# Optimization experiments

Hardware: AMD Instinct MI355X
Metric: run time of the kernel (lower is better)

## Reference

```python
import jax, jax.numpy as jnp
import numpy as np

B, S, D, H = 2, 4096, 512, 8
DH = D // H  # head dim = 64

def setup_inputs() -> dict:
    key = jax.random.key(0)
    ks = jax.random.split(key, 9)
    s = 0.02
    return {
        "Q": jax.random.normal(ks[0], (B, S, D), jnp.float32),
        "Wq": jax.random.normal(ks[1], (D, D), jnp.float32) * s,
        "bq": jnp.zeros((D,), jnp.float32),
        "Wk": jax.random.normal(ks[2], (D, D), jnp.float32) * s,
        "bk": jnp.zeros((D,), jnp.float32),
        "Wv": jax.random.normal(ks[3], (D, D), jnp.float32) * s,
        "bv": jnp.zeros((D,), jnp.float32),
        "Wo": jax.random.normal(ks[4], (D, D), jnp.float32) * s,
        "bo": jnp.zeros((D,), jnp.float32),
    }

def reference(Q, Wq, bq, Wk, bk, Wv, bv, Wo, bo):
    bs, s, d = Q.shape
    scale = DH ** -0.5
    # torch Linear: x @ W.T + b, W is [out, in]
    q = (Q @ Wq.T + bq).reshape(bs, s, H, DH).transpose(0, 2, 1, 3)  # [b,h,s,dh]
    k = (Q @ Wk.T + bk).reshape(bs, s, H, DH).transpose(0, 2, 1, 3)
    v = (Q @ Wv.T + bv).reshape(bs, s, H, DH).transpose(0, 2, 1, 3)
    scores = jnp.einsum('bhqd,bhkd->bhqk', q, k) * scale  # [b,h,s,s]
    attn = jax.nn.softmax(scores, axis=-1)
    out = jnp.einsum('bhqk,bhkd->bhqd', attn, v)  # [b,h,s,dh]
    out = out.transpose(0, 2, 1, 3).reshape(bs, s, H * DH)
    out = out @ Wo.T + bo
    return (out, attn)
```

## Files before the change

kernel.cpp:

```cpp
#include <hip/hip_runtime.h>
#include <hip/hip_bf16.h>

#define B_  2
#define S_  4096
#define D_  512
#define H_  8
#define DH_ 64
#define BH_ 16
#define M_  (B_*S_)

typedef __attribute__((ext_vector_type(4))) float f32x4;
typedef __attribute__((ext_vector_type(8))) short s16x8;
typedef __attribute__((ext_vector_type(4))) short s16x4;

#define MFMA(A,Bv,C) __builtin_amdgcn_mfma_f32_16x16x32_bf16(A,Bv,C,0,0,0)

typedef const void __attribute__((address_space(1)))* gas_t;
typedef void __attribute__((address_space(3)))* las_t;
#define GLDS(gp, lp) __builtin_amdgcn_global_load_lds((gas_t)(gp), (las_t)(lp), 16, 0, 0)

#define EXP_C 0.18033688011112042f

static __device__ __forceinline__ unsigned short f2bf(float f){
    union { float f; unsigned int u; } v; v.f = f;
    unsigned int r = (v.u + 0x7FFFu + ((v.u >> 16) & 1u)) >> 16;
    return (unsigned short)r;
}
static __device__ __forceinline__ float bf2f(unsigned short b){
    union { unsigned int u; float f; } v; v.u = ((unsigned int)b) << 16;
    return v.f;
}

__global__ __launch_bounds__(256) void cvt_bf16(const float* __restrict__ src,
                                                unsigned short* __restrict__ dst, int n4){
    int i = blockIdx.x * 256 + threadIdx.x;
    if (i < n4){
        float4 v = reinterpret_cast<const float4*>(src)[i];
        ushort4 o;
        o.x = f2bf(v.x); o.y = f2bf(v.y); o.z = f2bf(v.z); o.w = f2bf(v.w);
        reinterpret_cast<ushort4*>(dst)[i] = o;
    }
}

__global__ __launch_bounds__(256) void cvt_w4(const float* __restrict__ s0, const float* __restrict__ s1,
                                              const float* __restrict__ s2, const float* __restrict__ s3,
                                              unsigned short* __restrict__ d0, unsigned short* __restrict__ d1,
                                              unsigned short* __restrict__ d2, unsigned short* __restrict__ d3){
    const float* s; unsigned short* d;
    switch (blockIdx.y){
        case 0: s = s0; d = d0; break;
        case 1: s = s1; d = d1; break;
        case 2: s = s2; d = d2; break;
        default: s = s3; d = d3; break;
    }
    int i = blockIdx.x * 256 + threadIdx.x;
    float4 v = reinterpret_cast<const float4*>(s)[i];
    ushort4 o;
    o.x = f2bf(v.x); o.y = f2bf(v.y); o.z = f2bf(v.z); o.w = f2bf(v.w);
    reinterpret_cast<ushort4*>(d)[i] = o;
}

__global__ __launch_bounds__(256) void gemm_bt(const unsigned short* __restrict__ A,
                                               const unsigned short* __restrict__ W,
                                               const float* __restrict__ bias,
                                               unsigned short* __restrict__ dst_bf,
                                               float* __restrict__ dst_f32){
    const int mt = blockIdx.x, nt0 = blockIdx.y;
    const int wave = threadIdx.x >> 6, lane = threadIdx.x & 63;
    const int g = lane >> 4, r16 = lane & 15;
    const unsigned short* Ap = A + (size_t)(mt*64 + wave*16 + r16) * 512;

    f32x4 acc[4];
    #pragma unroll
    for (int i = 0; i < 4; ++i) acc[i] = (f32x4){0.f,0.f,0.f,0.f};

    #pragma unroll
    for (int k0 = 0; k0 < 512; k0 += 64){
        s16x8 a0 = *(const s16x8*)(Ap + k0 + g*8);
        s16x8 a1 = *(const s16x8*)(Ap + k0 + 32 + g*8);
        #pragma unroll
        for (int nt = 0; nt < 4; ++nt){
            const unsigned short* Wp = W + (size_t)(nt0*64 + nt*16 + r16)*512 + k0 + g*8;
            s16x8 b0 = *(const s16x8*)(Wp);
            s16x8 b1 = *(const s16x8*)(Wp + 32);
            acc[nt] = MFMA(a0, b0, acc[nt]);
            acc[nt] = MFMA(a1, b1, acc[nt]);
        }
    }

    #pragma unroll
    for (int nt = 0; nt < 4; ++nt){
        const int col = nt0*64 + nt*16 + r16;
        const float bv = bias[col];
        #pragma unroll
        for (int r = 0; r < 4; ++r){
            const int orow = mt*64 + wave*16 + g*4 + r;
            float val = acc[nt][r] + bv;
            if (dst_f32){
                dst_f32[(size_t)orow*512 + col] = val;
            } else {
                const int b = orow >> 12, s = orow & 4095;
                const int h = col >> 6,  dh = col & 63;
                dst_bf[((size_t)(b*H_ + h)*S_ + s)*DH_ + dh] = f2bf(val);
            }
        }
    }
}

__global__ __launch_bounds__(256) void transpose_v(const unsigned short* __restrict__ vh,
                                                   unsigned short* __restrict__ vT){
    __shared__ unsigned short tile[64][65];
    const int bh = blockIdx.y, s0 = blockIdx.x * 64;
    const int t = threadIdx.x, c = t & 63, r4 = t >> 6;
    const unsigned short* src = vh + (size_t)bh*S_*DH_;
    #pragma unroll
    for (int i = 0; i < 16; ++i){
        int sr = i*4 + r4;
        tile[sr][c] = src[(size_t)(s0 + sr)*DH_ + c];
    }
    __syncthreads();
    unsigned short* dst = vT + (size_t)bh*DH_*S_;
    #pragma unroll
    for (int i = 0; i < 16; ++i){
        int d = i*4 + r4;
        dst[(size_t)d*S_ + s0 + c] = tile[c][d];
    }
}

__global__ __launch_bounds__(512, 4) void attn_fused(const unsigned short* __restrict__ qh,
                                                     const unsigned short* __restrict__ kh,
                                                     const unsigned short* __restrict__ vT,
                                                     float* __restrict__ attn,
                                                     unsigned short* __restrict__ ctx){
    __shared__ unsigned short Kb[2][64][64];
    __shared__ unsigned short Vb[2][64][64];
    __shared__ __align__(16) unsigned short Pbf[8][16][136];

    const int lin = blockIdx.y * 32 + blockIdx.x;
    const int nl  = (lin & 7) * 64 + (lin >> 3);
    const int qt  = nl & 31;
    const int bh  = nl >> 5;

    const int wave = threadIdx.x >> 6, lane = threadIdx.x & 63;
    const int g = lane >> 4, r16 = lane & 15;

    const unsigned short* qbase = qh + (size_t)bh*S_*DH_;
    const unsigned short* kbase = kh + (size_t)bh*S_*DH_;
    const unsigned short* vbase = vT + (size_t)bh*DH_*S_;

    const int tr = wave*8 + (lane >> 3);
    const int cc = (lane & 7) ^ (tr & 7);
    unsigned short* kl[2] = { &Kb[0][wave*8][0], &Kb[1][wave*8][0] };
    unsigned short* vl[2] = { &Vb[0][wave*8][0], &Vb[1][wave*8][0] };

    const int sw = r16 & 7;
    const int c0 = (g ^ sw) * 8;
    const int c1 = ((4 + g) ^ sw) * 8;

    const int qrow = qt*128 + wave*16 + r16;
    s16x8 qa0 = *(const s16x8*)(qbase + (size_t)qrow*DH_ + g*8);
    s16x8 qa1 = *(const s16x8*)(qbase + (size_t)qrow*DH_ + 32 + g*8);

    GLDS(kbase + (size_t)tr*DH_ + cc*8, kl[0]);
    asm volatile("s_waitcnt vmcnt(0)" ::: "memory");
    __builtin_amdgcn_s_barrier();
    __builtin_amdgcn_sched_barrier(0);

    float lsum[4] = {0.f,0.f,0.f,0.f};
    for (int t = 0; t < 64; ++t){
        const int nxt = (t + 1) & 63;
        GLDS(kbase + (size_t)(nxt*64 + tr)*DH_ + cc*8, kl[(t&1)^1]);
        __builtin_amdgcn_sched_barrier(0);
        const unsigned short (*Kt)[64] = Kb[t&1];
        #pragma unroll
        for (int nt = 0; nt < 4; ++nt){
            const int row = nt*16 + r16;
            s16x8 b0 = *(const s16x8*)(&Kt[row][c0]);
            s16x8 b1 = *(const s16x8*)(&Kt[row][c1]);
            f32x4 acc = (f32x4){0.f,0.f,0.f,0.f};
            acc = MFMA(qa0, b0, acc);
            acc = MFMA(qa1, b1, acc);
            #pragma unroll
            for (int r = 0; r < 4; ++r)
                lsum[r] += __builtin_amdgcn_exp2f(acc[r]*EXP_C);
        }
        asm volatile("s_waitcnt vmcnt(0)" ::: "memory");
        __builtin_amdgcn_s_barrier();
        __builtin_amdgcn_sched_barrier(0);
    }

    #pragma unroll
    for (int m = 1; m < 16; m <<= 1){
        #pragma unroll
        for (int r = 0; r < 4; ++r) lsum[r] += __shfl_xor(lsum[r], m, 64);
    }
    float inv[4];
    #pragma unroll
    for (int r = 0; r < 4; ++r) inv[r] = 1.0f / lsum[r];

    f32x4 oacc[4];
    #pragma unroll
    for (int i = 0; i < 4; ++i) oacc[i] = (f32x4){0.f,0.f,0.f,0.f};

    GLDS(vbase + (size_t)tr*S_ + cc*8, vl[0]);
    asm volatile("s_waitcnt vmcnt(0)" ::: "memory");
    __builtin_amdgcn_s_barrier();
    __builtin_amdgcn_sched_barrier(0);

    float* attnW = attn + ((size_t)bh*S_ + qt*128 + wave*16)*S_;
    unsigned short (*Pw)[136] = Pbf[wave];
    const int sl = lane & 31, sh = lane >> 5;

    auto compute_tile = [&](int t){
        const unsigned short (*Kt)[64] = Kb[t&1];
        const unsigned short (*Vt)[64] = Vb[t&1];
        const int cb = (t&1)*64;
        f32x4 pacc[4];
        #pragma unroll
        for (int nt = 0; nt < 4; ++nt){
            const int row = nt*16 + r16;
            s16x8 b0 = *(const s16x8*)(&Kt[row][c0]);
            s16x8 b1 = *(const s16x8*)(&Kt[row][c1]);
            f32x4 acc = (f32x4){0.f,0.f,0.f,0.f};
            acc = MFMA(qa0, b0, acc);
            acc = MFMA(qa1, b1, acc);
            pacc[nt] = acc;
        }
        #pragma unroll
        for (int nt = 0; nt < 4; ++nt){
            #pragma unroll
            for (int r = 0; r < 4; ++r){
                float p = __builtin_amdgcn_exp2f(pacc[nt][r]*EXP_C) * inv[r];
                Pw[g*4 + r][cb + nt*16 + r16] = f2bf(p);
            }
        }
        s16x8 pa0 = *(const s16x8*)(&Pw[r16][cb + g*8]);
        s16x8 pa1 = *(const s16x8*)(&Pw[r16][cb + 32 + g*8]);
        #pragma unroll
        for (int nt = 0; nt < 4; ++nt){
            const int row = nt*16 + r16;
            s16x8 v0 = *(const s16x8*)(&Vt[row][c0]);
            s16x8 v1 = *(const s16x8*)(&Vt[row][c1]);
            oacc[nt] = MFMA(pa0, v0, oacc[nt]);
            oacc[nt] = MFMA(pa1, v1, oacc[nt]);
        }
    };

    auto store_pair = [&](int tfirst){
        #pragma unroll
        for (int i = 0; i < 8; ++i){
            const int row = i*2 + sh;
            s16x4 pb = *(const s16x4*)(&Pw[row][sl*4]);
            f32x4 o;
            #pragma unroll
            for (int j = 0; j < 4; ++j) o[j] = bf2f((unsigned short)pb[j]);
            __builtin_nontemporal_store(o,
                (f32x4*)(attnW + (size_t)row*S_ + tfirst*64 + sl*4));
        }
    };

    GLDS(kbase + (size_t)(1*64 + tr)*DH_ + cc*8, kl[1]);
    GLDS(vbase + (size_t)tr*S_ + 1*64 + cc*8,    vl[1]);
    __builtin_amdgcn_sched_barrier(0);
    compute_tile(0);
    asm volatile("s_waitcnt vmcnt(0)" ::: "memory");
    __builtin_amdgcn_s_barrier();
    __builtin_amdgcn_sched_barrier(0);

    for (int t = 1; t < 64; ++t){
        const int nxt = (t + 1) & 63;
        GLDS(kbase + (size_t)(nxt*64 + tr)*DH_ + cc*8, kl[(t&1)^1]);
        GLDS(vbase + (size_t)tr*S_ + nxt*64 + cc*8,    vl[(t&1)^1]);
        __builtin_amdgcn_sched_barrier(0);
        if ((t & 1) == 0){
            store_pair(t - 2);
            __builtin_amdgcn_sched_barrier(0);
        }
        compute_tile(t);
        if (t & 1){
            asm volatile("s_waitcnt vmcnt(0)" ::: "memory");
        } else {
            asm volatile("s_waitcnt vmcnt(8)" ::: "memory");
        }
        __builtin_amdgcn_s_barrier();
        __builtin_amdgcn_sched_barrier(0);
    }
    store_pair(62);

    const int b = bh >> 3, h = bh & 7;
    #pragma unroll
    for (int nt = 0; nt < 4; ++nt){
        #pragma unroll
        for (int r = 0; r < 4; ++r){
            const int qr = qt*128 + wave*16 + g*4 + r;
            ctx[(size_t)(b*S_ + qr)*D_ + h*64 + nt*16 + r16] = f2bf(oacc[nt][r]);
        }
    }
}

extern "C" void kernel_launch(void* const* d_in, const int* in_sizes, int n_in,
                              void* d_out, int out_size, void* d_ws, size_t ws_size,
                              hipStream_t stream){
    const float* Q  = (const float*)d_in[0];
    const float* Wq = (const float*)d_in[1];
    const float* bq = (const float*)d_in[2];
    const float* Wk = (const float*)d_in[3];
    const float* bk = (const float*)d_in[4];
    const float* Wv = (const float*)d_in[5];
    const float* bv = (const float*)d_in[6];
    const float* Wo = (const float*)d_in[7];
    const float* bo = (const float*)d_in[8];

    float* out  = (float*)d_out;
    float* attn = out + (size_t)M_*D_;

    unsigned short* Qbf = (unsigned short*)attn;
    unsigned short* Wqb = Qbf + (size_t)M_*D_;
    unsigned short* Wkb = Wqb + 512*512;
    unsigned short* Wvb = Wkb + 512*512;
    unsigned short* vh  = Wvb + 512*512;

    unsigned short* qhb = (unsigned short*)d_ws;
    unsigned short* khb = qhb + (size_t)BH_*S_*DH_;
    unsigned short* vTb = khb + (size_t)BH_*S_*DH_;
    unsigned short* ctx = vTb + (size_t)BH_*S_*DH_;
    unsigned short* Wob = ctx + (size_t)M_*D_;

    cvt_bf16<<<dim3(M_*D_/4/256), 256, 0, stream>>>(Q, Qbf, M_*D_/4);
    cvt_w4<<<dim3(512*512/4/256, 4), 256, 0, stream>>>(Wq, Wk, Wv, Wo, Wqb, Wkb, Wvb, Wob);

    dim3 pg(M_/64, D_/64);
    gemm_bt<<<pg, 256, 0, stream>>>(Qbf, Wqb, bq, qhb, nullptr);
    gemm_bt<<<pg, 256, 0, stream>>>(Qbf, Wkb, bk, khb, nullptr);
    gemm_bt<<<pg, 256, 0, stream>>>(Qbf, Wvb, bv, vh,  nullptr);

    transpose_v<<<dim3(S_/64, BH_), 256, 0, stream>>>(vh, vTb);

    attn_fused<<<dim3(32, BH_), 512, 0, stream>>>(qhb, khb, vTb, attn, ctx);

    gemm_bt<<<pg, 256, 0, stream>>>(ctx, Wob, bo, nullptr, out);
}
```

Before: 392.1 us.

## Fuse conversions, QKV projections with V transpose, and triple-buffer K in pass one

Merges the Q and weight bf16 conversion kernels into one launch. Fuses the three QKV projection GEMMs and the V transpose into one kernel that writes vT directly through shared memory. The first softmax-denominator pass in the attention kernel now uses a three-stage K buffer with a partial vmcnt wait, and the second pass's initial K/V loads are merged. It also switches f2bf to the HIP intrinsic. The aim is fewer launches and less global traffic, plus better latency hiding, at the cost of more shared memory and a serial per-block loop over three weights.

```diff
diff --git a/kernel.cpp b/kernel.cpp
--- a/kernel.cpp
+++ b/kernel.cpp
@@ -22,49 +22,109 @@
 #define EXP_C 0.18033688011112042f
 
 static __device__ __forceinline__ unsigned short f2bf(float f){
-    union { float f; unsigned int u; } v; v.f = f;
-    unsigned int r = (v.u + 0x7FFFu + ((v.u >> 16) & 1u)) >> 16;
-    return (unsigned short)r;
+    union { __hip_bfloat16 h; unsigned short u; } v;
+    v.h = __float2bfloat16(f);
+    return v.u;
 }
 static __device__ __forceinline__ float bf2f(unsigned short b){
     union { unsigned int u; float f; } v; v.u = ((unsigned int)b) << 16;
     return v.f;
 }
 
-__global__ __launch_bounds__(256) void cvt_bf16(const float* __restrict__ src,
-                                                unsigned short* __restrict__ dst, int n4){
+__global__ __launch_bounds__(256) void cvt_all(const float* __restrict__ Q,
+                                               const float* __restrict__ W0, const float* __restrict__ W1,
+                                               const float* __restrict__ W2, const float* __restrict__ W3,
+                                               unsigned short* __restrict__ Qd,
+                                               unsigned short* __restrict__ D0, unsigned short* __restrict__ D1,
+                                               unsigned short* __restrict__ D2, unsigned short* __restrict__ D3){
     int i = blockIdx.x * 256 + threadIdx.x;
-    if (i < n4){
-        float4 v = reinterpret_cast<const float4*>(src)[i];
-        ushort4 o;
-        o.x = f2bf(v.x); o.y = f2bf(v.y); o.z = f2bf(v.z); o.w = f2bf(v.w);
-        reinterpret_cast<ushort4*>(dst)[i] = o;
-    }
-}
-
-__global__ __launch_bounds__(256) void cvt_w4(const float* __restrict__ s0, const float* __restrict__ s1,
-                                              const float* __restrict__ s2, const float* __restrict__ s3,
-                                              unsigned short* __restrict__ d0, unsigned short* __restrict__ d1,
-                                              unsigned short* __restrict__ d2, unsigned short* __restrict__ d3){
-    const float* s; unsigned short* d;
-    switch (blockIdx.y){
-        case 0: s = s0; d = d0; break;
-        case 1: s = s1; d = d1; break;
-        case 2: s = s2; d = d2; break;
-        default: s = s3; d = d3; break;
-    }
-    int i = blockIdx.x * 256 + threadIdx.x;
-    float4 v = reinterpret_cast<const float4*>(s)[i];
+    const float* s; unsigned short* d; int off;
+    if (i < 1048576){ s = Q; d = Qd; off = i; }
+    else {
+        int j = i - 1048576;
+        int w = j >> 16; off = j & 65535;
+        s = (w==0)?W0:(w==1)?W1:(w==2)?W2:W3;
+        d = (w==0)?D0:(w==1)?D1:(w==2)?D2:D3;
+    }
+    float4 v = reinterpret_cast<const float4*>(s)[off];
     ushort4 o;
     o.x = f2bf(v.x); o.y = f2bf(v.y); o.z = f2bf(v.z); o.w = f2bf(v.w);
-    reinterpret_cast<ushort4*>(d)[i] = o;
+    reinterpret_cast<ushort4*>(d)[off] = o;
+}
+
+__global__ __launch_bounds__(256) void gemm_qkv(const unsigned short* __restrict__ A,
+                                                const unsigned short* __restrict__ Wq, const float* __restrict__ bq,
+                                                const unsigned short* __restrict__ Wk, const float* __restrict__ bk,
+                                                const unsigned short* __restrict__ Wv, const float* __restrict__ bv,
+                                                unsigned short* __restrict__ qh, unsigned short* __restrict__ kh,
+                                                unsigned short* __restrict__ vT){
+    __shared__ unsigned short tile[64][65];
+    const int mt = blockIdx.x, nt0 = blockIdx.y;
+    const int wave = threadIdx.x >> 6, lane = threadIdx.x & 63;
+    const int g = lane >> 4, r16 = lane & 15;
+    const unsigned short* Ap = A + (size_t)(mt*64 + wave*16 + r16) * 512;
+    const int b  = mt >> 6;
+    const int s0 = (mt & 63) * 64;
+    const int h  = nt0;
+
+    #pragma unroll 1
+    for (int w = 0; w < 3; ++w){
+        const unsigned short* W = (w==0)?Wq:(w==1)?Wk:Wv;
+        const float* bias       = (w==0)?bq:(w==1)?bk:bv;
+
+        f32x4 acc[4];
+        #pragma unroll
+        for (int i = 0; i < 4; ++i) acc[i] = (f32x4){0.f,0.f,0.f,0.f};
+
+        #pragma unroll
+        for (int k0 = 0; k0 < 512; k0 += 64){
+            s16x8 a0 = *(const s16x8*)(Ap + k0 + g*8);
+            s16x8 a1 = *(const s16x8*)(Ap + k0 + 32 + g*8);
+            #pragma unroll
+            for (int nt = 0; nt < 4; ++nt){
+                const unsigned short* Wp = W + (size_t)(nt0*64 + nt*16 + r16)*512 + k0 + g*8;
+                s16x8 b0 = *(const s16x8*)(Wp);
+                s16x8 b1 = *(const s16x8*)(Wp + 32);
+                acc[nt] = MFMA(a0, b0, acc[nt]);
+                acc[nt] = MFMA(a1, b1, acc[nt]);
+            }
+        }
+
+        if (w < 2){
+            unsigned short* dst = (w==0) ? qh : kh;
+            #pragma unroll
+            for (int nt = 0; nt < 4; ++nt){
+                const float bv_ = bias[nt0*64 + nt*16 + r16];
+                #pragma unroll
+                for (int r = 0; r < 4; ++r){
+                    const int s = s0 + wave*16 + g*4 + r;
+                    dst[((size_t)(b*H_ + h)*S_ + s)*DH_ + nt*16 + r16] = f2bf(acc[nt][r] + bv_);
+                }
+            }
+        } else {
+            #pragma unroll
+            for (int nt = 0; nt < 4; ++nt){
+                const float bv_ = bias[nt0*64 + nt*16 + r16];
+                #pragma unroll
+                for (int r = 0; r < 4; ++r)
+                    tile[wave*16 + g*4 + r][nt*16 + r16] = f2bf(acc[nt][r] + bv_);
+            }
+            __syncthreads();
+            const int c = threadIdx.x & 63, r4 = threadIdx.x >> 6;
+            unsigned short* dst = vT + (size_t)(b*H_ + h)*DH_*S_;
+            #pragma unroll
+            for (int i = 0; i < 16; ++i){
+                const int dh = i*4 + r4;
+                dst[(size_t)dh*S_ + s0 + c] = tile[c][dh];
+            }
+        }
+    }
 }
 
 __global__ __launch_bounds__(256) void gemm_bt(const unsigned short* __restrict__ A,
                                                const unsigned short* __restrict__ W,
                                                const float* __restrict__ bias,
-                                               unsigned short* __restrict__ dst_bf,
-                                               float* __restrict__ dst_f32){
+                                               float* __restrict__ dst){
     const int mt = blockIdx.x, nt0 = blockIdx.y;
     const int wave = threadIdx.x >> 6, lane = threadIdx.x & 63;
     const int g = lane >> 4, r16 = lane & 15;
@@ -90,40 +150,12 @@
 
     #pragma unroll
     for (int nt = 0; nt < 4; ++nt){
-        const int col = nt0*64 + nt*16 + r16;
-        const float bv = bias[col];
+        const float bv = bias[nt0*64 + nt*16 + r16];
         #pragma unroll
         for (int r = 0; r < 4; ++r){
             const int orow = mt*64 + wave*16 + g*4 + r;
-            float val = acc[nt][r] + bv;
-            if (dst_f32){
-                dst_f32[(size_t)orow*512 + col] = val;
-            } else {
-                const int b = orow >> 12, s = orow & 4095;
-                const int h = col >> 6,  dh = col & 63;
-                dst_bf[((size_t)(b*H_ + h)*S_ + s)*DH_ + dh] = f2bf(val);
-            }
-        }
-    }
-}
-
-__global__ __launch_bounds__(256) void transpose_v(const unsigned short* __restrict__ vh,
-                                                   unsigned short* __restrict__ vT){
-    __shared__ unsigned short tile[64][65];
-    const int bh = blockIdx.y, s0 = blockIdx.x * 64;
-    const int t = threadIdx.x, c = t & 63, r4 = t >> 6;
-    const unsigned short* src = vh + (size_t)bh*S_*DH_;
-    #pragma unroll
-    for (int i = 0; i < 16; ++i){
-        int sr = i*4 + r4;
-        tile[sr][c] = src[(size_t)(s0 + sr)*DH_ + c];
-    }
-    __syncthreads();
-    unsigned short* dst = vT + (size_t)bh*DH_*S_;
-    #pragma unroll
-    for (int i = 0; i < 16; ++i){
-        int d = i*4 + r4;
-        dst[(size_t)d*S_ + s0 + c] = tile[c][d];
+            dst[(size_t)orow*512 + nt0*64 + nt*16 + r16] = acc[nt][r] + bv;
+        }
     }
 }
 
@@ -132,7 +164,7 @@
                                                      const unsigned short* __restrict__ vT,
                                                      float* __restrict__ attn,
                                                      unsigned short* __restrict__ ctx){
-    __shared__ unsigned short Kb[2][64][64];
+    __shared__ unsigned short Kb[3*64*64];
     __shared__ unsigned short Vb[2][64][64];
     __shared__ __align__(16) unsigned short Pbf[8][16][136];
 
@@ -150,8 +182,7 @@
 
     const int tr = wave*8 + (lane >> 3);
     const int cc = (lane & 7) ^ (tr & 7);
-    unsigned short* kl[2] = { &Kb[0][wave*8][0], &Kb[1][wave*8][0] };
-    unsigned short* vl[2] = { &Vb[0][wave*8][0], &Vb[1][wave*8][0] };
+    const int stg = tr*64 + (lane & 7)*8;
 
     const int sw = r16 & 7;
     const int c0 = (g ^ sw) * 8;
@@ -161,66 +192,70 @@
     s16x8 qa0 = *(const s16x8*)(qbase + (size_t)qrow*DH_ + g*8);
     s16x8 qa1 = *(const s16x8*)(qbase + (size_t)qrow*DH_ + 32 + g*8);
 
-    GLDS(kbase + (size_t)tr*DH_ + cc*8, kl[0]);
+    GLDS(kbase + (size_t)tr*DH_ + cc*8,          Kb + 0*4096 + stg);
+    GLDS(kbase + (size_t)(64 + tr)*DH_ + cc*8,   Kb + 1*4096 + stg);
+
+    float lsum[4] = {0.f,0.f,0.f,0.f};
+    for (int t = 0; t < 64; ++t){
+        if (t == 63) asm volatile("s_waitcnt vmcnt(0)" ::: "memory");
+        else         asm volatile("s_waitcnt vmcnt(1)" ::: "memory");
+        __builtin_amdgcn_s_barrier();
+        __builtin_amdgcn_sched_barrier(0);
+        if (t < 62){
+            const int s2 = (t + 2) % 3;
+            GLDS(kbase + (size_t)((t+2)*64 + tr)*DH_ + cc*8, Kb + s2*4096 + stg);
+        }
+        __builtin_amdgcn_sched_barrier(0);
+        const unsigned short* Kt = Kb + (t % 3)*4096;
+        #pragma unroll
+        for (int nt = 0; nt < 4; ++nt){
+            const int row = nt*16 + r16;
+            s16x8 b0 = *(const s16x8*)(Kt + row*64 + c0);
+            s16x8 b1 = *(const s16x8*)(Kt + row*64 + c1);
+            f32x4 acc = (f32x4){0.f,0.f,0.f,0.f};
+            acc = MFMA(qa0, b0, acc);
+            acc = MFMA(qa1, b1, acc);
+            #pragma unroll
+            for (int r = 0; r < 4; ++r)
+                lsum[r] += __builtin_amdgcn_exp2f(acc[r]*EXP_C);
+        }
+    }
+
+    #pragma unroll
+    for (int m = 1; m < 16; m <<= 1){
+        #pragma unroll
+        for (int r = 0; r < 4; ++r) lsum[r] += __shfl_xor(lsum[r], m, 64);
+    }
+    float inv[4];
+    #pragma unroll
+    for (int r = 0; r < 4; ++r) inv[r] = 1.0f / lsum[r];
+
+    __builtin_amdgcn_s_barrier();
+    __builtin_amdgcn_sched_barrier(0);
+    GLDS(kbase + (size_t)tr*DH_ + cc*8, Kb + 0*4096 + stg);
+    GLDS(vbase + (size_t)tr*S_  + cc*8, &Vb[0][0][0] + stg);
     asm volatile("s_waitcnt vmcnt(0)" ::: "memory");
     __builtin_amdgcn_s_barrier();
     __builtin_amdgcn_sched_barrier(0);
 
-    float lsum[4] = {0.f,0.f,0.f,0.f};
-    for (int t = 0; t < 64; ++t){
-        const int nxt = (t + 1) & 63;
-        GLDS(kbase + (size_t)(nxt*64 + tr)*DH_ + cc*8, kl[(t&1)^1]);
-        __builtin_amdgcn_sched_barrier(0);
-        const unsigned short (*Kt)[64] = Kb[t&1];
-        #pragma unroll
-        for (int nt = 0; nt < 4; ++nt){
-            const int row = nt*16 + r16;
-            s16x8 b0 = *(const s16x8*)(&Kt[row][c0]);
-            s16x8 b1 = *(const s16x8*)(&Kt[row][c1]);
-            f32x4 acc = (f32x4){0.f,0.f,0.f,0.f};
-            acc = MFMA(qa0, b0, acc);
-            acc = MFMA(qa1, b1, acc);
-            #pragma unroll
-            for (int r = 0; r < 4; ++r)
-                lsum[r] += __builtin_amdgcn_exp2f(acc[r]*EXP_C);
-        }
-        asm volatile("s_waitcnt vmcnt(0)" ::: "memory");
-        __builtin_amdgcn_s_barrier();
-        __builtin_amdgcn_sched_barrier(0);
-    }
-
-    #pragma unroll
-    for (int m = 1; m < 16; m <<= 1){
-        #pragma unroll
-        for (int r = 0; r < 4; ++r) lsum[r] += __shfl_xor(lsum[r], m, 64);
-    }
-    float inv[4];
-    #pragma unroll
-    for (int r = 0; r < 4; ++r) inv[r] = 1.0f / lsum[r];
-
     f32x4 oacc[4];
     #pragma unroll
     for (int i = 0; i < 4; ++i) oacc[i] = (f32x4){0.f,0.f,0.f,0.f};
-
-    GLDS(vbase + (size_t)tr*S_ + cc*8, vl[0]);
-    asm volatile("s_waitcnt vmcnt(0)" ::: "memory");
-    __builtin_amdgcn_s_barrier();
-    __builtin_amdgcn_sched_barrier(0);
 
     float* attnW = attn + ((size_t)bh*S_ + qt*128 + wave*16)*S_;
     unsigned short (*Pw)[136] = Pbf[wave];
     const int sl = lane & 31, sh = lane >> 5;
 
     auto compute_tile = [&](int t){
-        const unsigned short (*Kt)[64] = Kb[t&1];
+        const unsigned short* Kt = Kb + (t&1)*4096;
         const unsigned short (*Vt)[64] = Vb[t&1];
         const int cb = (t&1)*64;
         f32x4 pacc[4];
         #pragma unroll
         for (int nt = 0; nt < 4; ++nt){
             const int row = nt*16 + r16;
-            s16x8 b0 = *(const s16x8*)(&Kt[row][c0]);
-            s16x8 b1 = *(const s16x8*)(&Kt[row][c1]);
+            s16x8 b0 = *(const s16x8*)(Kt + row*64 + c0);
+            s16x8 b1 = *(const s16x8*)(Kt + row*64 + c1);
             f32x4 acc = (f32x4){0.f,0.f,0.f,0.f};
             acc = MFMA(qa0, b0, acc);
             acc = MFMA(qa1, b1, acc);
@@ -259,8 +294,8 @@
         }
     };
 
-    GLDS(kbase + (size_t)(1*64 + tr)*DH_ + cc*8, kl[1]);
-    GLDS(vbase + (size_t)tr*S_ + 1*64 + cc*8,    vl[1]);
+    GLDS(kbase + (size_t)(1*64 + tr)*DH_ + cc*8, Kb + 1*4096 + stg);
+    GLDS(vbase + (size_t)tr*S_ + 1*64 + cc*8,    &Vb[1][0][0] + stg);
     __builtin_amdgcn_sched_barrier(0);
     compute_tile(0);
     asm volatile("s_waitcnt vmcnt(0)" ::: "memory");
@@ -269,8 +304,8 @@
 
     for (int t = 1; t < 64; ++t){
         const int nxt = (t + 1) & 63;
-        GLDS(kbase + (size_t)(nxt*64 + tr)*DH_ + cc*8, kl[(t&1)^1]);
-        GLDS(vbase + (size_t)tr*S_ + nxt*64 + cc*8,    vl[(t&1)^1]);
+        GLDS(kbase + (size_t)(nxt*64 + tr)*DH_ + cc*8, Kb + ((t&1)^1)*4096 + stg);
+        GLDS(vbase + (size_t)tr*S_ + nxt*64 + cc*8,    &Vb[(t&1)^1][0][0] + stg);
         __builtin_amdgcn_sched_barrier(0);
         if ((t & 1) == 0){
             store_pair(t - 2);
@@ -318,7 +353,6 @@
     unsigned short* Wqb = Qbf + (size_t)M_*D_;
     unsigned short* Wkb = Wqb + 512*512;
     unsigned short* Wvb = Wkb + 512*512;
-    unsigned short* vh  = Wvb + 512*512;
 
     unsigned short* qhb = (unsigned short*)d_ws;
     unsigned short* khb = qhb + (size_t)BH_*S_*DH_;
@@ -326,17 +360,12 @@
     unsigned short* ctx = vTb + (size_t)BH_*S_*DH_;
     unsigned short* Wob = ctx + (size_t)M_*D_;
 
-    cvt_bf16<<<dim3(M_*D_/4/256), 256, 0, stream>>>(Q, Qbf, M_*D_/4);
-    cvt_w4<<<dim3(512*512/4/256, 4), 256, 0, stream>>>(Wq, Wk, Wv, Wo, Wqb, Wkb, Wvb, Wob);
-
-    dim3 pg(M_/64, D_/64);
-    gemm_bt<<<pg, 256, 0, stream>>>(Qbf, Wqb, bq, qhb, nullptr);
-    gemm_bt<<<pg, 256, 0, stream>>>(Qbf, Wkb, bk, khb, nullptr);
-    gemm_bt<<<pg, 256, 0, stream>>>(Qbf, Wvb, bv, vh,  nullptr);
-
-    transpose_v<<<dim3(S_/64, BH_), 256, 0, stream>>>(vh, vTb);
+    cvt_all<<<dim3(5120), 256, 0, stream>>>(Q, Wq, Wk, Wv, Wo, Qbf, Wqb, Wkb, Wvb, Wob);
+
+    gemm_qkv<<<dim3(M_/64, 8), 256, 0, stream>>>(Qbf, Wqb, bq, Wkb, bk, Wvb, bv,
+                                                 qhb, khb, vTb);
 
     attn_fused<<<dim3(32, BH_), 512, 0, stream>>>(qhb, khb, vTb, attn, ctx);
 
-    gemm_bt<<<pg, 256, 0, stream>>>(ctx, Wob, bo, nullptr, out);
-}
+    gemm_bt<<<dim3(M_/64, D_/64), 256, 0, stream>>>(ctx, Wob, bo, out);
+}
```

Result: faster. 377.3 us (median of 3 runs) (-3.8%).
